# Optimization experiments

Measured on AMD Instinct MI355X. Metric: run time of the kernel, lower is better.

Reference implementation:

```python
import jax, jax.numpy as jnp
import numpy as np

# Block-sparse linear config: W is (OUT_F, IN_F) in BSR form with BS x BS blocks,
OUT_F, IN_F, BS, K = 4096, 4096, 64, 32
NROW, NCOL = OUT_F // BS, IN_F // BS   # 64, 64
NNZB = NROW * K                         # 2048 nonzero blocks
BATCH = 8192


def setup_inputs() -> dict:
    key = jax.random.key(0)
    k1, k2, k3 = jax.random.split(key, 3)
    x = jax.random.normal(k1, (BATCH, IN_F), jnp.float32)
    values = jax.random.normal(k2, (NNZB, BS, BS), jnp.float32) * 0.02
    bias = jax.random.normal(k3, (OUT_F,), jnp.float32) * 0.01
    # BSR structure: K sorted, distinct column-block indices per block-row.
    cols = np.stack([np.sort((r + 2 * np.arange(K)) % NCOL) for r in range(NROW)])
    col_indices = jnp.asarray(cols.reshape(-1), jnp.int32)          # [NNZB]
    crow_indices = jnp.arange(NROW + 1, dtype=jnp.int32) * K        # [NROW+1]
    return {"x": x, "values": values, "bias": bias,
            "crow_indices": crow_indices, "col_indices": col_indices}


def reference(x, values, bias, crow_indices, col_indices):
    # Expand BSR row pointers to per-block row ids (structure is static/int).
    counts = jnp.diff(crow_indices)
    row_ids = jnp.repeat(jnp.arange(NROW), counts, total_repeat_length=NNZB)
    # Scatter nonzero blocks into a dense weight (only ~67 MB, cheap vs the GEMM).
    Wb = jnp.zeros((NROW, NCOL, BS, BS), values.dtype).at[row_ids, col_indices].set(values)
    W = Wb.transpose(0, 2, 1, 3).reshape(OUT_F, IN_F)  # [out_features, in_features]
    # forward: (W @ x.T).T + bias  ==  x @ W.T + bias
    return x @ W.T + bias
```

## Files before the change

kernel.cpp:

```cpp
#include <hip/hip_runtime.h>
#include <stdint.h>


#define BATCH   8192
#define IN_F    4096
#define OUT_F   4096
#define BS      64
#define NROW    64
#define NNZB    2048
#define BM      256
#define LDS_A_BYTES (BM * BS * 2)
#define LDS_B_BYTES (2 * BS * BS * 2)

typedef float f32x4 __attribute__((ext_vector_type(4)));
typedef short s16x8 __attribute__((ext_vector_type(8)));

__device__ __forceinline__ void async_copy16(const void* g, void* l) {
  __builtin_amdgcn_global_load_lds(
      (__attribute__((address_space(1))) void*)g,
      (__attribute__((address_space(3))) void*)l, 16, 0, 0);
}

__device__ __forceinline__ unsigned short f32_to_bf16(float f) {
  union { float f; uint32_t u; } v; v.f = f;
  return (unsigned short)((v.u + 0x7FFFu + ((v.u >> 16) & 1u)) >> 16);
}

__global__ void cvt_kernel(const float4* __restrict__ in,
                           ushort4* __restrict__ out, int n4) {
  int i = blockIdx.x * blockDim.x + threadIdx.x;
  if (i < n4) {
    float4 v = in[i];
    ushort4 o;
    o.x = f32_to_bf16(v.x); o.y = f32_to_bf16(v.y);
    o.z = f32_to_bf16(v.z); o.w = f32_to_bf16(v.w);
    out[i] = o;
  }
}

__global__ __launch_bounds__(512) void bsr_gemm_pair_kernel(
    const unsigned short* __restrict__ xb,
    const unsigned short* __restrict__ wb,
    const float* __restrict__ bias,
    const int* __restrict__ crow,
    const int* __restrict__ cols,
    float* __restrict__ out) {
  __shared__ alignas(16) char smem[LDS_A_BYTES + LDS_B_BYTES];

  const int tid = threadIdx.x;
  const int w   = tid >> 6;
  const int l   = tid & 63;
  const int wm  = w & 3;
  const int wn  = w >> 2;
  const int p   = blockIdx.x;
  const int rA  = ((p >> 1) << 2) + (p & 1);
  const int rB  = rA + 2;
  const int m0  = blockIdx.y * BM;

  const int startA = crow[rA], endA = crow[rA + 1];
  const int startB = crow[rB], endB = crow[rB + 1];

  const int lr = l & 15;
  const int q  = l >> 4;

  int cvA = (startA + l < endA) ? cols[startA + l] : 0;
  int cvB = (startB + l < endB) ? cols[startB + l] : 0;

  f32x4 acc[4][4];
#pragma unroll
  for (int mi = 0; mi < 4; ++mi)
#pragma unroll
    for (int ni = 0; ni < 4; ++ni) {
      f32x4 z = {0.f, 0.f, 0.f, 0.f};
      acc[mi][ni] = z;
    }

  const int srow = tid >> 3;
  const int sswz = ((tid & 7) ^ (srow & 7)) << 3;
  const unsigned short* agbase =
      xb + (size_t)(m0 + srow) * IN_F + sswz;
  char* const alds = smem + tid * 16;
  char* const blds = smem + LDS_A_BYTES + tid * 16;
  const int bgoff = (srow << 6) + sswz;

  int ia = startA, ib = startB;
  while ((ia < endA) || (ib < endB)) {
    const int ca = (ia < endA) ? __shfl(cvA, ia - startA) : 0x7fffffff;
    const int cb = (ib < endB) ? __shfl(cvB, ib - startB) : 0x7fffffff;
    const int c = min(ca, cb);
    const bool hasA = (ca == c);
    const bool hasB = (cb == c);
    const int iA = ia, iB = ib;
    if (hasA) ++ia;
    if (hasB) ++ib;

    __syncthreads();
    const unsigned short* ag = agbase + (size_t)c * BS;
#pragma unroll
    for (int it = 0; it < 4; ++it)
      async_copy16(ag + (size_t)(it * 64) * IN_F, alds + it * 8192);
    if (hasA)
      async_copy16(wb + ((size_t)iA << 12) + bgoff, blds);
    if (hasB)
      async_copy16(wb + ((size_t)iB << 12) + bgoff, blds + 8192);
    __syncthreads();

    const bool active = wn ? hasB : hasA;
    if (active) {
#pragma unroll
      for (int ks = 0; ks < 2; ++ks) {
        const int chunk = (((ks << 2) + q) ^ (l & 7)) << 4;
        s16x8 af[4], bf[4];
#pragma unroll
        for (int mi = 0; mi < 4; ++mi)
          af[mi] = *(const s16x8*)(smem +
                     ((wm << 6) + (mi << 4) + lr) * 128 + chunk);
#pragma unroll
        for (int ni = 0; ni < 4; ++ni)
          bf[ni] = *(const s16x8*)(smem + LDS_A_BYTES + (wn << 13) +
                     ((ni << 4) + lr) * 128 + chunk);
#pragma unroll
        for (int mi = 0; mi < 4; ++mi)
#pragma unroll
          for (int ni = 0; ni < 4; ++ni)
            acc[mi][ni] = __builtin_amdgcn_mfma_f32_16x16x32_bf16(
                af[mi], bf[ni], acc[mi][ni], 0, 0, 0);
      }
    }
  }

  const int rW = wn ? rB : rA;
  const int colg = (rW << 6) + lr;
#pragma unroll
  for (int ni = 0; ni < 4; ++ni) {
    const float bv = bias[colg + (ni << 4)];
#pragma unroll
    for (int mi = 0; mi < 4; ++mi) {
      float* op = out +
          (size_t)(m0 + (wm << 6) + (mi << 4) + (q << 2)) * OUT_F +
          colg + (ni << 4);
#pragma unroll
      for (int e = 0; e < 4; ++e)
        op[(size_t)e * OUT_F] = acc[mi][ni][e] + bv;
    }
  }
}

__global__ void fallback_kernel(const float* __restrict__ x,
                                const float* __restrict__ vals,
                                const float* __restrict__ bias,
                                const int* __restrict__ crow,
                                const int* __restrict__ cols,
                                float* __restrict__ out) {
  int idx = blockIdx.x * 256 + threadIdx.x;
  int m = idx >> 12;
  int n = idx & 4095;
  int r = n >> 6, nl = n & 63;
  float s = 0.f;
  int e = crow[r + 1];
  for (int i = crow[r]; i < e; ++i) {
    const float* xp = x + (size_t)m * IN_F + cols[i] * 64;
    const float* wp = vals + ((size_t)i << 12) + nl * 64;
    for (int k = 0; k < 64; ++k) s += xp[k] * wp[k];
  }
  out[idx] = s + bias[n];
}

extern "C" void kernel_launch(void* const* d_in, const int* in_sizes, int n_in,
                              void* d_out, int out_size, void* d_ws,
                              size_t ws_size, hipStream_t stream) {
  const float* x    = (const float*)d_in[0];
  const float* vals = (const float*)d_in[1];
  const float* bias = (const float*)d_in[2];
  const int*   crow = (const int*)d_in[3];
  const int*   cols = (const int*)d_in[4];
  float* out = (float*)d_out;

  const size_t x_elems = (size_t)BATCH * IN_F;
  const size_t w_elems = (size_t)NNZB * BS * BS;
  const size_t need = (x_elems + w_elems) * 2;

  if (ws_size >= need) {
    unsigned short* xb = (unsigned short*)d_ws;
    unsigned short* wb = xb + x_elems;
    cvt_kernel<<<(int)(x_elems / 4 / 256), 256, 0, stream>>>(
        (const float4*)x, (ushort4*)xb, (int)(x_elems / 4));
    cvt_kernel<<<(int)(w_elems / 4 / 256), 256, 0, stream>>>(
        (const float4*)vals, (ushort4*)wb, (int)(w_elems / 4));
    dim3 grid(NROW / 2, BATCH / BM);
    bsr_gemm_pair_kernel<<<grid, 512, 0, stream>>>(xb, wb, bias, crow, cols,
                                                   out);
  } else {
    fallback_kernel<<<(BATCH * OUT_F) / 256, 256, 0, stream>>>(
        x, vals, bias, crow, cols, out);
  }
}
```

Measured before the change: 370.5 us.

## Double-buffer LDS tiles with a precomputed merged column schedule; fuse conversion kernels

The GEMM kernel now precomputes the merged column-block schedule for the two block-rows into per-lane registers. It then double-buffers the A and B tiles in LDS, so the next step's async global-to-LDS loads overlap the current step's MFMA work, and it needs one barrier per step instead of two. It also raises wave priority during the MFMA section and merges the two bf16 conversion launches into one. The cost is double the LDS (96 KB), which may lower occupancy, plus redundant B loads when one row lacks a block. The schedule is held one step per lane, so it assumes at most 64 merged steps.

Measured after the change: 418.5 us. +13.0%, slower.

```diff
diff --git a/kernel.cpp b/kernel.cpp
--- a/kernel.cpp
+++ b/kernel.cpp
@@ -9,8 +9,10 @@
 #define NROW    64
 #define NNZB    2048
 #define BM      256
-#define LDS_A_BYTES (BM * BS * 2)
-#define LDS_B_BYTES (2 * BS * BS * 2)
+#define LDS_A_BYTES 32768
+#define LDS_B_BYTES 16384
+#define BUF_BYTES   (LDS_A_BYTES + LDS_B_BYTES)
+#define NBUF    2
 
 typedef float f32x4 __attribute__((ext_vector_type(4)));
 typedef short s16x8 __attribute__((ext_vector_type(8)));
@@ -26,16 +28,20 @@
   return (unsigned short)((v.u + 0x7FFFu + ((v.u >> 16) & 1u)) >> 16);
 }
 
-__global__ void cvt_kernel(const float4* __restrict__ in,
-                           ushort4* __restrict__ out, int n4) {
+__global__ void cvt_kernel(const float4* __restrict__ xin,
+                           const float4* __restrict__ win,
+                           ushort4* __restrict__ xout,
+                           ushort4* __restrict__ wout, int nx4, int ntot4) {
   int i = blockIdx.x * blockDim.x + threadIdx.x;
-  if (i < n4) {
-    float4 v = in[i];
-    ushort4 o;
-    o.x = f32_to_bf16(v.x); o.y = f32_to_bf16(v.y);
-    o.z = f32_to_bf16(v.z); o.w = f32_to_bf16(v.w);
-    out[i] = o;
-  }
+  if (i >= ntot4) return;
+  const float4* src; ushort4* dst; int j;
+  if (i < nx4) { src = xin; dst = xout; j = i; }
+  else         { src = win; dst = wout; j = i - nx4; }
+  float4 v = src[j];
+  ushort4 o;
+  o.x = f32_to_bf16(v.x); o.y = f32_to_bf16(v.y);
+  o.z = f32_to_bf16(v.z); o.w = f32_to_bf16(v.w);
+  dst[j] = o;
 }
 
 __global__ __launch_bounds__(512) void bsr_gemm_pair_kernel(
@@ -45,7 +51,7 @@
     const int* __restrict__ crow,
     const int* __restrict__ cols,
     float* __restrict__ out) {
-  __shared__ alignas(16) char smem[LDS_A_BYTES + LDS_B_BYTES];
+  __shared__ alignas(16) char smem[NBUF * BUF_BYTES];
 
   const int tid = threadIdx.x;
   const int w   = tid >> 6;
@@ -66,6 +72,25 @@
   int cvA = (startA + l < endA) ? cols[startA + l] : 0;
   int cvB = (startB + l < endB) ? cols[startB + l] : 0;
 
+  int myc = 0, mypk = 0;
+  int nt = 0;
+  {
+    int ia = startA, ib = startB;
+    const int clA = (endA > startA) ? endA - 1 : 0;
+    const int clB = (endB > startB) ? endB - 1 : 0;
+    while ((ia < endA) || (ib < endB)) {
+      const int ca = (ia < endA) ? __shfl(cvA, ia - startA) : 0x7fffffff;
+      const int cb = (ib < endB) ? __shfl(cvB, ib - startB) : 0x7fffffff;
+      const int c  = min(ca, cb);
+      const int hA = (ca == c);
+      const int hB = (cb == c);
+      const int sA = hA ? ia : clA;
+      const int sB = hB ? ib : clB;
+      if (nt == l) { myc = c; mypk = sA | (sB << 12) | (hA << 24) | (hB << 25); }
+      ia += hA; ib += hB; ++nt;
+    }
+  }
+
   f32x4 acc[4][4];
 #pragma unroll
   for (int mi = 0; mi < 4; ++mi)
@@ -79,45 +104,44 @@
   const int sswz = ((tid & 7) ^ (srow & 7)) << 3;
   const unsigned short* agbase =
       xb + (size_t)(m0 + srow) * IN_F + sswz;
-  char* const alds = smem + tid * 16;
-  char* const blds = smem + LDS_A_BYTES + tid * 16;
   const int bgoff = (srow << 6) + sswz;
 
-  int ia = startA, ib = startB;
-  while ((ia < endA) || (ib < endB)) {
-    const int ca = (ia < endA) ? __shfl(cvA, ia - startA) : 0x7fffffff;
-    const int cb = (ib < endB) ? __shfl(cvB, ib - startB) : 0x7fffffff;
-    const int c = min(ca, cb);
-    const bool hasA = (ca == c);
-    const bool hasB = (cb == c);
-    const int iA = ia, iB = ib;
-    if (hasA) ++ia;
-    if (hasB) ++ib;
-
-    __syncthreads();
+  auto stage = [&](int t, int buf) {
+    const int c  = __shfl(myc, t);
+    const int pk = __shfl(mypk, t);
+    const int sA = pk & 0xfff;
+    const int sB = (pk >> 12) & 0xfff;
+    char* const al = smem + buf * BUF_BYTES + tid * 16;
+    char* const bl = smem + buf * BUF_BYTES + LDS_A_BYTES + tid * 16;
     const unsigned short* ag = agbase + (size_t)c * BS;
 #pragma unroll
     for (int it = 0; it < 4; ++it)
-      async_copy16(ag + (size_t)(it * 64) * IN_F, alds + it * 8192);
-    if (hasA)
-      async_copy16(wb + ((size_t)iA << 12) + bgoff, blds);
-    if (hasB)
-      async_copy16(wb + ((size_t)iB << 12) + bgoff, blds + 8192);
-    __syncthreads();
-
-    const bool active = wn ? hasB : hasA;
-    if (active) {
+      async_copy16(ag + (size_t)(it * 64) * IN_F, al + it * 8192);
+    async_copy16(wb + ((size_t)sA << 12) + bgoff, bl);
+    async_copy16(wb + ((size_t)sB << 12) + bgoff, bl + 8192);
+  };
+
+  if (nt > 0) stage(0, 0);
+  __syncthreads();
+  int cur = 0;
+  for (int t = 0; t < nt; ++t) {
+    if (t + 1 < nt) stage(t + 1, cur ^ 1);
+
+    const int pk = __shfl(mypk, t);
+    const char* const cbase = smem + cur * BUF_BYTES;
+    if ((pk >> (24 + wn)) & 1) {
+      __builtin_amdgcn_s_setprio(1);
 #pragma unroll
       for (int ks = 0; ks < 2; ++ks) {
         const int chunk = (((ks << 2) + q) ^ (l & 7)) << 4;
         s16x8 af[4], bf[4];
 #pragma unroll
         for (int mi = 0; mi < 4; ++mi)
-          af[mi] = *(const s16x8*)(smem +
+          af[mi] = *(const s16x8*)(cbase +
                      ((wm << 6) + (mi << 4) + lr) * 128 + chunk);
 #pragma unroll
         for (int ni = 0; ni < 4; ++ni)
-          bf[ni] = *(const s16x8*)(smem + LDS_A_BYTES + (wn << 13) +
+          bf[ni] = *(const s16x8*)(cbase + LDS_A_BYTES + (wn << 13) +
                      ((ni << 4) + lr) * 128 + chunk);
 #pragma unroll
         for (int mi = 0; mi < 4; ++mi)
@@ -126,7 +150,10 @@
             acc[mi][ni] = __builtin_amdgcn_mfma_f32_16x16x32_bf16(
                 af[mi], bf[ni], acc[mi][ni], 0, 0, 0);
       }
-    }
+      __builtin_amdgcn_s_setprio(0);
+    }
+    __syncthreads();
+    cur ^= 1;
   }
 
   const int rW = wn ? rB : rA;
@@ -182,13 +209,14 @@
 
   if (ws_size >= need) {
     unsigned short* xb = (unsigned short*)d_ws;
-    unsigned short* wb = xb + x_elems;
-    cvt_kernel<<<(int)(x_elems / 4 / 256), 256, 0, stream>>>(
-        (const float4*)x, (ushort4*)xb, (int)(x_elems / 4));
-    cvt_kernel<<<(int)(w_elems / 4 / 256), 256, 0, stream>>>(
-        (const float4*)vals, (ushort4*)wb, (int)(w_elems / 4));
+    unsigned short* wbp = xb + x_elems;
+    const int nx4 = (int)(x_elems / 4);
+    const int ntot4 = (int)((x_elems + w_elems) / 4);
+    cvt_kernel<<<(ntot4 + 255) / 256, 256, 0, stream>>>(
+        (const float4*)x, (const float4*)vals,
+        (ushort4*)xb, (ushort4*)wbp, nx4, ntot4);
     dim3 grid(NROW / 2, BATCH / BM);
-    bsr_gemm_pair_kernel<<<grid, 512, 0, stream>>>(xb, wb, bias, crow, cols,
+    bsr_gemm_pair_kernel<<<grid, 512, 0, stream>>>(xb, wbp, bias, crow, cols,
                                                    out);
   } else {
     fallback_kernel<<<(BATCH * OUT_F) / 256, 256, 0, stream>>>(
```
